# Optimization experiments

Measured on AMD Instinct MI355X. Metric: run time of the kernel, lower is better.

The kernel has to match this reference:

```python
import jax, jax.numpy as jnp
import numpy as np

# --- config (matches init_kwargs) ---
NUM_EXPERTS = 8
TOP_K = 2
GROUP_DET = 1024
GROUP_CLS = 512
D_MODEL = 768
MLP_DIM = 3072


def setup_inputs() -> dict:
    key = jax.random.key(0)
    ks = jax.random.split(key, 8)
    scale = 0.02
    return {
        "x_det": jax.random.normal(ks[0], (16, 1024, D_MODEL), dtype=jnp.float32),
        "x_cls": jax.random.normal(ks[1], (16, 256, D_MODEL), dtype=jnp.float32),
        "w_router_det": jax.random.normal(ks[2], (D_MODEL, NUM_EXPERTS), dtype=jnp.float32) * scale,
        "w_router_cls": jax.random.normal(ks[3], (D_MODEL, NUM_EXPERTS), dtype=jnp.float32) * scale,
        "w1": jax.random.normal(ks[4], (NUM_EXPERTS, D_MODEL, MLP_DIM), dtype=jnp.float32) * scale,
        "b1": jnp.zeros((NUM_EXPERTS, MLP_DIM), dtype=jnp.float32),
        "w2": jax.random.normal(ks[5], (NUM_EXPERTS, MLP_DIM, D_MODEL), dtype=jnp.float32) * scale,
        "b2": jnp.zeros((NUM_EXPERTS, D_MODEL), dtype=jnp.float32),
    }


def _route(xg, w_router, top_k, num_experts, capacity):
    """Top-k per-item routing with expert capacity (vmoe-style einsum dispatcher).

    xg: [G, S, D] grouped tokens. Returns dispatch [G,S,E,C], combine [G,S,E,C].
    """
    G, S, _ = xg.shape
    gates = jax.nn.softmax(jnp.einsum("gsd,de->gse", xg, w_router))  # [G,S,E]
    gval, gidx = jax.lax.top_k(gates, top_k)  # [G,S,k]
    # k-major ordering: slot-0 choices of all tokens get capacity priority.
    mask = jax.nn.one_hot(gidx, num_experts, dtype=xg.dtype)  # [G,S,k,E]
    mask = mask.transpose(0, 2, 1, 3).reshape(G, top_k * S, num_experts)
    pos = jnp.cumsum(mask, axis=1) - 1.0  # position within expert buffer
    keep = mask * (pos < capacity)
    disp = keep[..., None] * jax.nn.one_hot(pos, capacity, dtype=xg.dtype)  # [G,kS,E,C]
    disp = disp.reshape(G, top_k, S, num_experts, capacity)
    combine = jnp.einsum("gksec,gks->gsec", disp, gval.transpose(0, 2, 1))
    dispatch = disp.sum(axis=1)  # [G,S,E,C] (one-hot: a token goes to each expert <=1 time)
    return dispatch, combine


def _expert_mlp(expert_in, w1, b1, w2, b2):
    # expert_in: [E, N, D] -> vmapped-expert MLP (grouped GEMM)
    h = jax.nn.gelu(jnp.einsum("end,edh->enh", expert_in, w1) + b1[:, None, :])
    return jnp.einsum("enh,ehd->end", h, w2) + b2[:, None, :]


def _moe(x, w_router, w1, b1, w2, b2, group_size):
    B, S, D = x.shape
    G = (B * S) // group_size
    capacity = (TOP_K * group_size) // NUM_EXPERTS
    xg = x.reshape(G, group_size, D)
    dispatch, combine = _route(xg, w_router, TOP_K, NUM_EXPERTS, capacity)
    expert_in = jnp.einsum("gsec,gsd->egcd", dispatch, xg)  # [E,G,C,D]
    E, _, C, _ = expert_in.shape
    y = _expert_mlp(expert_in.reshape(E, G * C, D), w1, b1, w2, b2).reshape(E, G, C, D)
    out = jnp.einsum("gsec,egcd->gsd", combine, y)
    return out.reshape(B, S, D)


def reference(x_det, x_cls, w_router_det, w_router_cls, w1, b1, w2, b2):
    out_det = _moe(x_det, w_router_det, w1, b1, w2, b2, GROUP_DET)
    out_cls = _moe(x_cls, w_router_cls, w1, b1, w2, b2, GROUP_CLS)
    # concatenate the two streams along the sequence axis for a single output
    return jnp.concatenate([out_det, out_cls], axis=1)
```

## Files before the change

kernel.cpp:

```cpp
#include <hip/hip_runtime.h>
#include <cstdint>
#include <cstddef>

#define NE 8
#define DMODEL 768
#define MLPDIM 3072
#define NDET 16384
#define NCLS 4096
#define NTOK 20480
#define ROWS_PER_E 5120
#define TOT_ROWS 40960

typedef float f32x4 __attribute__((ext_vector_type(4)));
typedef __bf16 bf16x8 __attribute__((ext_vector_type(8)));

__device__ __forceinline__ unsigned short f2bf(float f) {
    unsigned u = __float_as_uint(f);
    u += 0x7FFFu + ((u >> 16) & 1u);
    return (unsigned short)(u >> 16);
}
__device__ __forceinline__ float bf2f(unsigned v) {
    return __uint_as_float(v << 16);
}
__device__ __forceinline__ float gelu_f(float x) {
    float u = 0.7978845608028654f * (x + 0.044715f * x * x * x);
    float t = __expf(-2.0f * fabsf(u));
    float th = __builtin_copysignf((1.0f - t) * __frcp_rn(1.0f + t), u);
    return 0.5f * x * (1.0f + th);
}

__device__ __forceinline__ void gload16(const void* g, void* l) {
    __builtin_amdgcn_global_load_lds(
        (const __attribute__((address_space(1))) unsigned int*)g,
        (__attribute__((address_space(3))) unsigned int*)l, 16, 0, 0);
}

__global__ void k_router(const float* __restrict__ xd, const float* __restrict__ xc,
                         const float* __restrict__ wrd, const float* __restrict__ wrc,
                         ushort* __restrict__ xbf,
                         int* __restrict__ e1, int* __restrict__ e2,
                         float* __restrict__ g1, float* __restrict__ g2) {
    int wave = threadIdx.x >> 6, lane = threadIdx.x & 63;
    int t = blockIdx.x * 4 + wave;
    if (t >= NTOK) return;
    const float* xrow;
    const float* w;
    if (t < NDET) { xrow = xd + (size_t)t * DMODEL; w = wrd; }
    else          { xrow = xc + (size_t)(t - NDET) * DMODEL; w = wrc; }
    ushort* xbrow = xbf + (size_t)t * DMODEL;
    float acc[8];
    #pragma unroll
    for (int e = 0; e < 8; e++) acc[e] = 0.0f;
    #pragma unroll
    for (int kk = 0; kk < DMODEL / 64; kk++) {
        int k = kk * 64 + lane;
        float xv = xrow[k];
        xbrow[k] = f2bf(xv);
        const float* wr = w + k * 8;
        #pragma unroll
        for (int e = 0; e < 8; e++) acc[e] += xv * wr[e];
    }
    #pragma unroll
    for (int e = 0; e < 8; e++) {
        #pragma unroll
        for (int off = 32; off > 0; off >>= 1) acc[e] += __shfl_xor(acc[e], off);
    }
    int i1 = 0; float v1 = acc[0];
    #pragma unroll
    for (int e = 1; e < 8; e++) if (acc[e] > v1) { v1 = acc[e]; i1 = e; }
    int i2 = -1; float v2 = -1e30f;
    #pragma unroll
    for (int e = 0; e < 8; e++) if (e != i1 && acc[e] > v2) { v2 = acc[e]; i2 = e; }
    float Z = 0.0f;
    #pragma unroll
    for (int e = 0; e < 8; e++) Z += __expf(acc[e] - v1);
    if (lane == 0) {
        e1[t] = i1; e2[t] = i2;
        g1[t] = 1.0f / Z;
        g2[t] = __expf(v2 - v1) / Z;
    }
}

__global__ void k_transpose_bf(const float* __restrict__ in, ushort* __restrict__ out,
                               int K, int N) {
    __shared__ float tile[32][33];
    int e = blockIdx.z;
    const float* A = in + (size_t)e * K * N;
    ushort* B = out + (size_t)e * N * K;
    int n0 = blockIdx.x * 32, k0 = blockIdx.y * 32;
    int tx = threadIdx.x, ty = threadIdx.y;
    float4 v = *(const float4*)(A + (size_t)(k0 + ty) * N + n0 + tx * 4);
    tile[ty][tx * 4 + 0] = v.x; tile[ty][tx * 4 + 1] = v.y;
    tile[ty][tx * 4 + 2] = v.z; tile[ty][tx * 4 + 3] = v.w;
    __syncthreads();
    ushort4 o;
    o.x = f2bf(tile[tx * 4 + 0][ty]);
    o.y = f2bf(tile[tx * 4 + 1][ty]);
    o.z = f2bf(tile[tx * 4 + 2][ty]);
    o.w = f2bf(tile[tx * 4 + 3][ty]);
    *(ushort4*)(B + (size_t)(n0 + ty) * K + k0 + tx * 4) = o;
}

__global__ void k_scan(const int* __restrict__ e1, const int* __restrict__ e2,
                       int* __restrict__ slot_map, int* __restrict__ r1, int* __restrict__ r2) {
    int g = blockIdx.x;
    int lane = threadIdx.x;
    int S, C, base;
    if (g < 16) { S = 1024; C = 256; base = g * 1024; }
    else        { S = 512;  C = 128; base = NDET + (g - 16) * 512; }
    int cnt[8];
    #pragma unroll
    for (int e = 0; e < 8; e++) cnt[e] = 0;
    unsigned long long lower = (lane == 0) ? 0ULL : ((~0ULL) >> (64 - lane));
    int nch = (2 * S) >> 6;
    for (int ch = 0; ch < nch; ch++) {
        int n = ch * 64 + lane;
        int k = (n >= S) ? 1 : 0;
        int s = n - k * S;
        int tok = base + s;
        int e = k ? e2[tok] : e1[tok];
        int pos = 0;
        #pragma unroll
        for (int ee = 0; ee < 8; ee++) {
            unsigned long long m = __ballot(e == ee);
            if (e == ee) pos = cnt[ee] + __popcll(m & lower);
            cnt[ee] += __popcll(m);
        }
        int r = -1;
        if (pos < C) {
            int local = (g < 16) ? (g * 256 + pos) : (4096 + (g - 16) * 128 + pos);
            r = e * ROWS_PER_E + local;
            slot_map[r] = tok;
        }
        if (k == 0) r1[tok] = r; else r2[tok] = r;
    }
}

template<int KTOT, int NTOT, int MODE>
__global__ __launch_bounds__(512, 2) void k_gemm(
    const ushort* __restrict__ Asrc, const int* __restrict__ slot_map,
    const ushort* __restrict__ wtBase, const float* __restrict__ biasBase,
    ushort* __restrict__ Cdst, int eBase) {
    constexpr int KT = KTOT / 64;
    constexpr int NBN = NTOT / 256;
    __shared__ __align__(1024) ushort As[2][256 * 64];
    __shared__ __align__(1024) ushort Bs[2][256 * 64];

    const int q = gridDim.x >> 3;
    const int id2 = (blockIdx.x & 7) * q + (blockIdx.x >> 3);
    const int mb = id2 / NBN, nb = id2 - mb * NBN;
    const int e = eBase + mb / (ROWS_PER_E / 256);
    const int m0 = mb * 256;
    const int rbase = eBase * ROWS_PER_E + m0;
    const int n0 = nb * 256;
    const ushort* Bt = wtBase + (size_t)e * KTOT * NTOT;
    const float* bias = biasBase + (size_t)e * NTOT;

    const int t = threadIdx.x, lane = t & 63, wave = t >> 6;
    const int g8 = lane >> 3;
    const int p8 = lane & 7;
    const int swz = ((p8 ^ g8) << 4);

    const char* aS[4];
    const char* bS[4];
    #pragma unroll
    for (int j = 0; j < 4; j++) {
        int r = wave * 32 + j * 8 + g8;
        size_t arow;
        if (MODE == 0) { int tk = slot_map[rbase + r]; arow = (size_t)(tk < 0 ? 0 : tk); }
        else           { arow = (size_t)(m0 + r); }
        aS[j] = (const char*)(Asrc + arow * KTOT) + swz;
        bS[j] = (const char*)(Bt + (size_t)(n0 + r) * KTOT) + swz;
    }

    auto ISSUE = [&](int kt, int buf) {
        size_t o = (size_t)kt * 128;
        #pragma unroll
        for (int j = 0; j < 4; j++) {
            gload16(aS[j] + o, &As[buf][(wave * 32 + j * 8) * 64]);
            gload16(bS[j] + o, &Bs[buf][(wave * 32 + j * 8) * 64]);
        }
    };

    const int wr = wave >> 2, wc = wave & 3;
    const int l15 = lane & 15, kq = lane >> 4, l7 = lane & 7;

    f32x4 acc[8][4] = {};
    ISSUE(0, 0);
    int cur = 0;
    for (int kt = 0; kt < KT; ++kt) {
        __syncthreads();
        if (kt + 1 < KT) ISSUE(kt + 1, cur ^ 1);
        #pragma unroll
        for (int kc = 0; kc < 2; kc++) {
            const int ch = ((kq + 4 * kc) ^ l7) << 3;
            bf16x8 af[8], bfr[4];
            #pragma unroll
            for (int mf = 0; mf < 8; mf++)
                af[mf] = *(const bf16x8*)(&As[cur][(wr * 128 + mf * 16 + l15) * 64 + ch]);
            #pragma unroll
            for (int nf = 0; nf < 4; nf++)
                bfr[nf] = *(const bf16x8*)(&Bs[cur][(wc * 64 + nf * 16 + l15) * 64 + ch]);
            __builtin_amdgcn_s_setprio(1);
            #pragma unroll
            for (int mf = 0; mf < 8; mf++) {
                #pragma unroll
                for (int nf = 0; nf < 4; nf++)
                    acc[mf][nf] = __builtin_amdgcn_mfma_f32_16x16x32_bf16(af[mf], bfr[nf], acc[mf][nf], 0, 0, 0);
            }
            __builtin_amdgcn_s_setprio(0);
        }
        cur ^= 1;
    }

    const int ccolb = n0 + wc * 64 + l15;
    float bv[4];
    #pragma unroll
    for (int nf = 0; nf < 4; nf++) bv[nf] = bias[ccolb + nf * 16];

    const int rowb = (MODE == 0 ? m0 : rbase) + wr * 128 + (lane >> 4) * 4;
    #pragma unroll
    for (int mf = 0; mf < 8; mf++) {
        #pragma unroll
        for (int j = 0; j < 4; j++) {
            size_t roff = (size_t)(rowb + mf * 16 + j) * NTOT;
            #pragma unroll
            for (int nf = 0; nf < 4; nf++) {
                float v = acc[mf][nf][j] + bv[nf];
                if (MODE == 0) v = gelu_f(v);
                Cdst[roff + ccolb + nf * 16] = f2bf(v);
            }
        }
    }
}

__global__ void k_combine(const ushort* __restrict__ y,
                          const int* __restrict__ r1, const int* __restrict__ r2,
                          const float* __restrict__ g1, const float* __restrict__ g2,
                          float* __restrict__ out) {
    int t = blockIdx.x;
    int d = threadIdx.x;
    int a = r1[t], b = r2[t];
    float wa = g1[t], wb = g2[t];
    size_t opos;
    if (t < NDET) { int bb = t >> 10, s = t & 1023; opos = ((size_t)bb * 1280 + s) * 768; }
    else { int tt = t - NDET; int bb = tt >> 8, s = tt & 255; opos = ((size_t)bb * 1280 + 1024 + s) * 768; }
    int di = d * 4;
    float4 o = make_float4(0.f, 0.f, 0.f, 0.f);
    if (a >= 0) {
        uint2 v = *(const uint2*)(y + (size_t)a * 768 + di);
        o.x += wa * bf2f(v.x & 0xffffu); o.y += wa * bf2f(v.x >> 16);
        o.z += wa * bf2f(v.y & 0xffffu); o.w += wa * bf2f(v.y >> 16);
    }
    if (b >= 0) {
        uint2 v = *(const uint2*)(y + (size_t)b * 768 + di);
        o.x += wb * bf2f(v.x & 0xffffu); o.y += wb * bf2f(v.x >> 16);
        o.z += wb * bf2f(v.y & 0xffffu); o.w += wb * bf2f(v.y >> 16);
    }
    *(float4*)(out + opos + di) = o;
}

extern "C" void kernel_launch(void* const* d_in, const int* in_sizes, int n_in,
                              void* d_out, int out_size, void* d_ws, size_t ws_size,
                              hipStream_t stream) {
    const float* xd  = (const float*)d_in[0];
    const float* xc  = (const float*)d_in[1];
    const float* wrd = (const float*)d_in[2];
    const float* wrc = (const float*)d_in[3];
    const float* w1  = (const float*)d_in[4];
    const float* b1  = (const float*)d_in[5];
    const float* w2  = (const float*)d_in[6];
    const float* b2  = (const float*)d_in[7];
    float* out = (float*)d_out;

    size_t off = 0;
    char* base = (char*)d_ws;
    auto alloc = [&](size_t bytes) -> char* {
        char* r = base + off;
        off += (bytes + 255) & ~(size_t)255;
        return r;
    };
    ushort* xbf = (ushort*)alloc((size_t)NTOK * DMODEL * 2);
    ushort* w1t = (ushort*)alloc((size_t)NE * MLPDIM * DMODEL * 2);
    ushort* w2t = (ushort*)alloc((size_t)NE * DMODEL * MLPDIM * 2);
    ushort* y   = (ushort*)alloc((size_t)TOT_ROWS * DMODEL * 2);
    int*   slot_map = (int*)alloc((size_t)TOT_ROWS * 4);
    int*   e1 = (int*)alloc((size_t)NTOK * 4);
    int*   e2 = (int*)alloc((size_t)NTOK * 4);
    float* g1 = (float*)alloc((size_t)NTOK * 4);
    float* g2 = (float*)alloc((size_t)NTOK * 4);
    int*   r1 = (int*)alloc((size_t)NTOK * 4);
    int*   r2 = (int*)alloc((size_t)NTOK * 4);

    const size_t h_per_e = (size_t)ROWS_PER_E * MLPDIM * 2;
    int chunkE = 0;
    for (int c = NE; c >= 2; c >>= 1)
        if (off + c * h_per_e <= ws_size) { chunkE = c; break; }
    if (!chunkE) return;
    ushort* h = (ushort*)alloc((size_t)chunkE * h_per_e);

    hipMemsetAsync(slot_map, 0xFF, (size_t)TOT_ROWS * 4, stream);

    k_router<<<NTOK / 4, 256, 0, stream>>>(xd, xc, wrd, wrc, xbf, e1, e2, g1, g2);
    k_transpose_bf<<<dim3(MLPDIM / 32, DMODEL / 32, NE), dim3(8, 32), 0, stream>>>(w1, w1t, DMODEL, MLPDIM);
    k_transpose_bf<<<dim3(DMODEL / 32, MLPDIM / 32, NE), dim3(8, 32), 0, stream>>>(w2, w2t, MLPDIM, DMODEL);
    k_scan<<<24, 64, 0, stream>>>(e1, e2, slot_map, r1, r2);

    for (int e0 = 0; e0 < NE; e0 += chunkE) {
        int nmb = chunkE * (ROWS_PER_E / 256);
        k_gemm<DMODEL, MLPDIM, 0><<<nmb * (MLPDIM / 256), 512, 0, stream>>>(
            xbf, slot_map, w1t, b1, h, e0);
        k_gemm<MLPDIM, DMODEL, 1><<<nmb * (DMODEL / 256), 512, 0, stream>>>(
            h, slot_map, w2t, b2, y, e0);
    }

    k_combine<<<NTOK, 192, 0, stream>>>(y, r1, r2, g1, g2, out);
}
```

Measured before the change: 675.1 us.

## Restructure GEMM main loop with explicit waitcnt, phased LDS reads and prefetch distance two

Rewrites the GEMM K-loop to use four named LDS buffers, issue loads two tiles ahead, and wait with explicit vmcnt counters rather than a full __syncthreads. Each tile is split into four phases that read A fragments per phase and B once, separated by s_barrier and sched_barrier. The aim is to overlap global loads and LDS reads with MFMA work while using fewer fragment registers. The extra barriers per tile add synchronization overhead, and correctness depends on the hand-written vmcnt values.

```diff
diff --git a/kernel.cpp b/kernel.cpp
--- a/kernel.cpp
+++ b/kernel.cpp
@@ -143,8 +143,10 @@
     ushort* __restrict__ Cdst, int eBase) {
     constexpr int KT = KTOT / 64;
     constexpr int NBN = NTOT / 256;
-    __shared__ __align__(1024) ushort As[2][256 * 64];
-    __shared__ __align__(1024) ushort Bs[2][256 * 64];
+    __shared__ __align__(1024) ushort As0[256 * 64];
+    __shared__ __align__(1024) ushort As1[256 * 64];
+    __shared__ __align__(1024) ushort Bs0[256 * 64];
+    __shared__ __align__(1024) ushort Bs1[256 * 64];
 
     const int q = gridDim.x >> 3;
     const int id2 = (blockIdx.x & 7) * q + (blockIdx.x >> 3);
@@ -173,44 +175,71 @@
         bS[j] = (const char*)(Bt + (size_t)(n0 + r) * KTOT) + swz;
     }
 
-    auto ISSUE = [&](int kt, int buf) {
+    auto ISSUE = [&](int kt, ushort* SA, ushort* SB) {
         size_t o = (size_t)kt * 128;
         #pragma unroll
         for (int j = 0; j < 4; j++) {
-            gload16(aS[j] + o, &As[buf][(wave * 32 + j * 8) * 64]);
-            gload16(bS[j] + o, &Bs[buf][(wave * 32 + j * 8) * 64]);
+            gload16(aS[j] + o, SA + (wave * 32 + j * 8) * 64);
+            gload16(bS[j] + o, SB + (wave * 32 + j * 8) * 64);
         }
     };
 
     const int wr = wave >> 2, wc = wave & 3;
     const int l15 = lane & 15, kq = lane >> 4, l7 = lane & 7;
+    const int ch0 = ((kq) ^ l7) << 3;
+    const int ch1 = ((4 + kq) ^ l7) << 3;
 
     f32x4 acc[8][4] = {};
-    ISSUE(0, 0);
-    int cur = 0;
-    for (int kt = 0; kt < KT; ++kt) {
-        __syncthreads();
-        if (kt + 1 < KT) ISSUE(kt + 1, cur ^ 1);
-        #pragma unroll
-        for (int kc = 0; kc < 2; kc++) {
-            const int ch = ((kq + 4 * kc) ^ l7) << 3;
-            bf16x8 af[8], bfr[4];
+
+    auto TILE = [&](int kt, ushort* RA, ushort* RB) {
+        if (kt == KT - 1) { asm volatile("s_waitcnt vmcnt(0)" ::: "memory"); }
+        else              { asm volatile("s_waitcnt vmcnt(8)" ::: "memory"); }
+        __builtin_amdgcn_sched_barrier(0);
+        __builtin_amdgcn_s_barrier();
+        __builtin_amdgcn_sched_barrier(0);
+        bf16x8 bfr[4][2];
+        #pragma unroll
+        for (int p = 0; p < 4; ++p) {
+            bf16x8 af[2][2];
             #pragma unroll
-            for (int mf = 0; mf < 8; mf++)
-                af[mf] = *(const bf16x8*)(&As[cur][(wr * 128 + mf * 16 + l15) * 64 + ch]);
-            #pragma unroll
-            for (int nf = 0; nf < 4; nf++)
-                bfr[nf] = *(const bf16x8*)(&Bs[cur][(wc * 64 + nf * 16 + l15) * 64 + ch]);
+            for (int mi = 0; mi < 2; mi++) {
+                const int row = (wr * 128 + (2 * p + mi) * 16 + l15) * 64;
+                af[mi][0] = *(const bf16x8*)(&RA[row + ch0]);
+                af[mi][1] = *(const bf16x8*)(&RA[row + ch1]);
+            }
+            if (p == 0) {
+                #pragma unroll
+                for (int nf = 0; nf < 4; nf++) {
+                    const int row = (wc * 64 + nf * 16 + l15) * 64;
+                    bfr[nf][0] = *(const bf16x8*)(&RB[row + ch0]);
+                    bfr[nf][1] = *(const bf16x8*)(&RB[row + ch1]);
+                }
+            }
+            asm volatile("s_waitcnt lgkmcnt(0)" ::: "memory");
+            __builtin_amdgcn_sched_barrier(0);
             __builtin_amdgcn_s_setprio(1);
             #pragma unroll
-            for (int mf = 0; mf < 8; mf++) {
+            for (int kc = 0; kc < 2; kc++) {
                 #pragma unroll
-                for (int nf = 0; nf < 4; nf++)
-                    acc[mf][nf] = __builtin_amdgcn_mfma_f32_16x16x32_bf16(af[mf], bfr[nf], acc[mf][nf], 0, 0, 0);
+                for (int mi = 0; mi < 2; mi++) {
+                    #pragma unroll
+                    for (int nf = 0; nf < 4; nf++)
+                        acc[2 * p + mi][nf] = __builtin_amdgcn_mfma_f32_16x16x32_bf16(
+                            af[mi][kc], bfr[nf][kc], acc[2 * p + mi][nf], 0, 0, 0);
+                }
             }
             __builtin_amdgcn_s_setprio(0);
-        }
-        cur ^= 1;
+            __builtin_amdgcn_s_barrier();
+            __builtin_amdgcn_sched_barrier(0);
+        }
+        if (kt + 2 < KT) ISSUE(kt + 2, RA, RB);
+    };
+
+    ISSUE(0, As0, Bs0);
+    ISSUE(1, As1, Bs1);
+    for (int kt = 0; kt < KT; kt += 2) {
+        TILE(kt,     As0, Bs0);
+        TILE(kt + 1, As1, Bs1);
     }
 
     const int ccolb = n0 + wc * 64 + l15;
```

New measurement: 683.3 us. About the same (+1.2%).

## Shrink GEMM tiles to 128x128 with single-buffered LDS and split-k register prefetch

Applied to the files above, without the earlier changes.

Changes the expert GEMM from 256x256 tiles with 512 threads and double-buffered LDS to 128x128 tiles with 256 threads and a single LDS buffer. The second k-half fragments are loaded into registers before the next tile's global loads are issued, so the load overlaps the second half of the MFMAs. This lowers LDS and register use so more blocks fit per CU, at the cost of less data reuse per tile and an extra barrier per k-step.

```diff
diff --git a/kernel.cpp b/kernel.cpp
--- a/kernel.cpp
+++ b/kernel.cpp
@@ -137,22 +137,22 @@
 }
 
 template<int KTOT, int NTOT, int MODE>
-__global__ __launch_bounds__(512, 2) void k_gemm(
+__global__ __launch_bounds__(256, 4) void k_gemm(
     const ushort* __restrict__ Asrc, const int* __restrict__ slot_map,
     const ushort* __restrict__ wtBase, const float* __restrict__ biasBase,
     ushort* __restrict__ Cdst, int eBase) {
     constexpr int KT = KTOT / 64;
-    constexpr int NBN = NTOT / 256;
-    __shared__ __align__(1024) ushort As[2][256 * 64];
-    __shared__ __align__(1024) ushort Bs[2][256 * 64];
+    constexpr int NBN = NTOT / 128;
+    __shared__ __align__(1024) ushort As[128 * 64];
+    __shared__ __align__(1024) ushort Bs[128 * 64];
 
     const int q = gridDim.x >> 3;
     const int id2 = (blockIdx.x & 7) * q + (blockIdx.x >> 3);
     const int mb = id2 / NBN, nb = id2 - mb * NBN;
-    const int e = eBase + mb / (ROWS_PER_E / 256);
-    const int m0 = mb * 256;
+    const int e = eBase + mb / (ROWS_PER_E / 128);
+    const int m0 = mb * 128;
     const int rbase = eBase * ROWS_PER_E + m0;
-    const int n0 = nb * 256;
+    const int n0 = nb * 128;
     const ushort* Bt = wtBase + (size_t)e * KTOT * NTOT;
     const float* bias = biasBase + (size_t)e * NTOT;
 
@@ -173,44 +173,58 @@
         bS[j] = (const char*)(Bt + (size_t)(n0 + r) * KTOT) + swz;
     }
 
-    auto ISSUE = [&](int kt, int buf) {
+    auto ISSUE = [&](int kt) {
         size_t o = (size_t)kt * 128;
         #pragma unroll
         for (int j = 0; j < 4; j++) {
-            gload16(aS[j] + o, &As[buf][(wave * 32 + j * 8) * 64]);
-            gload16(bS[j] + o, &Bs[buf][(wave * 32 + j * 8) * 64]);
+            gload16(aS[j] + o, As + (wave * 32 + j * 8) * 64);
+            gload16(bS[j] + o, Bs + (wave * 32 + j * 8) * 64);
         }
     };
 
-    const int wr = wave >> 2, wc = wave & 3;
+    const int wr = wave >> 1, wc = wave & 1;
     const int l15 = lane & 15, kq = lane >> 4, l7 = lane & 7;
-
-    f32x4 acc[8][4] = {};
-    ISSUE(0, 0);
-    int cur = 0;
-    for (int kt = 0; kt < KT; ++kt) {
+    const int ch[2] = { ((kq) ^ l7) << 3, ((4 + kq) ^ l7) << 3 };
+
+    f32x4 acc[4][4] = {};
+
+    ISSUE(0);
+    for (int ks = 0; ks < KT; ks++) {
         __syncthreads();
-        if (kt + 1 < KT) ISSUE(kt + 1, cur ^ 1);
-        #pragma unroll
-        for (int kc = 0; kc < 2; kc++) {
-            const int ch = ((kq + 4 * kc) ^ l7) << 3;
-            bf16x8 af[8], bfr[4];
-            #pragma unroll
-            for (int mf = 0; mf < 8; mf++)
-                af[mf] = *(const bf16x8*)(&As[cur][(wr * 128 + mf * 16 + l15) * 64 + ch]);
+        bf16x8 af0[4], bf0[4];
+        #pragma unroll
+        for (int mi = 0; mi < 4; mi++)
+            af0[mi] = *(const bf16x8*)(&As[(wr * 64 + mi * 16 + l15) * 64 + ch[0]]);
+        #pragma unroll
+        for (int nf = 0; nf < 4; nf++)
+            bf0[nf] = *(const bf16x8*)(&Bs[(wc * 64 + nf * 16 + l15) * 64 + ch[0]]);
+        __builtin_amdgcn_s_setprio(1);
+        #pragma unroll
+        for (int mi = 0; mi < 4; mi++) {
             #pragma unroll
             for (int nf = 0; nf < 4; nf++)
-                bfr[nf] = *(const bf16x8*)(&Bs[cur][(wc * 64 + nf * 16 + l15) * 64 + ch]);
-            __builtin_amdgcn_s_setprio(1);
+                acc[mi][nf] = __builtin_amdgcn_mfma_f32_16x16x32_bf16(
+                    af0[mi], bf0[nf], acc[mi][nf], 0, 0, 0);
+        }
+        __builtin_amdgcn_s_setprio(0);
+        bf16x8 af1[4], bf1[4];
+        #pragma unroll
+        for (int mi = 0; mi < 4; mi++)
+            af1[mi] = *(const bf16x8*)(&As[(wr * 64 + mi * 16 + l15) * 64 + ch[1]]);
+        #pragma unroll
+        for (int nf = 0; nf < 4; nf++)
+            bf1[nf] = *(const bf16x8*)(&Bs[(wc * 64 + nf * 16 + l15) * 64 + ch[1]]);
+        __syncthreads();
+        if (ks + 1 < KT) ISSUE(ks + 1);
+        __builtin_amdgcn_s_setprio(1);
+        #pragma unroll
+        for (int mi = 0; mi < 4; mi++) {
             #pragma unroll
-            for (int mf = 0; mf < 8; mf++) {
-                #pragma unroll
-                for (int nf = 0; nf < 4; nf++)
-                    acc[mf][nf] = __builtin_amdgcn_mfma_f32_16x16x32_bf16(af[mf], bfr[nf], acc[mf][nf], 0, 0, 0);
-            }
-            __builtin_amdgcn_s_setprio(0);
-        }
-        cur ^= 1;
+            for (int nf = 0; nf < 4; nf++)
+                acc[mi][nf] = __builtin_amdgcn_mfma_f32_16x16x32_bf16(
+                    af1[mi], bf1[nf], acc[mi][nf], 0, 0, 0);
+        }
+        __builtin_amdgcn_s_setprio(0);
     }
 
     const int ccolb = n0 + wc * 64 + l15;
@@ -218,15 +232,15 @@
     #pragma unroll
     for (int nf = 0; nf < 4; nf++) bv[nf] = bias[ccolb + nf * 16];
 
-    const int rowb = (MODE == 0 ? m0 : rbase) + wr * 128 + (lane >> 4) * 4;
-    #pragma unroll
-    for (int mf = 0; mf < 8; mf++) {
+    const int rowb = (MODE == 0 ? m0 : rbase) + wr * 64 + (lane >> 4) * 4;
+    #pragma unroll
+    for (int mi = 0; mi < 4; mi++) {
         #pragma unroll
         for (int j = 0; j < 4; j++) {
-            size_t roff = (size_t)(rowb + mf * 16 + j) * NTOT;
+            size_t roff = (size_t)(rowb + mi * 16 + j) * NTOT;
             #pragma unroll
             for (int nf = 0; nf < 4; nf++) {
-                float v = acc[mf][nf][j] + bv[nf];
+                float v = acc[mi][nf][j] + bv[nf];
                 if (MODE == 0) v = gelu_f(v);
                 Cdst[roff + ccolb + nf * 16] = f2bf(v);
             }
@@ -307,10 +321,10 @@
     k_scan<<<24, 64, 0, stream>>>(e1, e2, slot_map, r1, r2);
 
     for (int e0 = 0; e0 < NE; e0 += chunkE) {
-        int nmb = chunkE * (ROWS_PER_E / 256);
-        k_gemm<DMODEL, MLPDIM, 0><<<nmb * (MLPDIM / 256), 512, 0, stream>>>(
+        int nmb = chunkE * (ROWS_PER_E / 128);
+        k_gemm<DMODEL, MLPDIM, 0><<<nmb * (MLPDIM / 128), 256, 0, stream>>>(
             xbf, slot_map, w1t, b1, h, e0);
-        k_gemm<MLPDIM, DMODEL, 1><<<nmb * (DMODEL / 256), 512, 0, stream>>>(
+        k_gemm<MLPDIM, DMODEL, 1><<<nmb * (DMODEL / 128), 256, 0, stream>>>(
             h, slot_map, w2t, b2, y, e0);
     }
 
```

Result: faster. 573.7 us (-15.0%).
